# Optimization experiments

Hardware: AMD Instinct MI355X
Metric: run time of the kernel (lower is better)

The kernel has to match this reference:

```python
import jax, jax.numpy as jnp
import numpy as np

B, T, V, L = 32, 1000, 1024, 128
BLANK = 0
NEG = -1e30  # log-space -inf surrogate (fp32 safe)


def setup_inputs() -> dict:
    key = jax.random.key(0)
    k1, k2 = jax.random.split(key)
    hs_pad = jax.random.normal(k1, (B, T, V), dtype=jnp.float32)
    h_lens = jnp.full((B,), T, dtype=jnp.int32)
    ys_pad = jax.random.randint(k2, (B, L), 1, V, dtype=jnp.int32)  # blank=0 excluded
    ys_lens = jnp.full((B,), L, dtype=jnp.int32)
    return {"hs_pad": hs_pad, "h_lens": h_lens, "ys_pad": ys_pad, "ys_lens": ys_lens}


def ctc_loss(hs_pad, h_lens, ys_pad, ys_lens):
    """log_softmax + CTC forward (alpha) DP, 'mean' reduction like torch.nn.CTCLoss."""
    logp = jax.nn.log_softmax(hs_pad, axis=-1)          # (B, T, V)
    Bsz, Tm, _ = hs_pad.shape
    Lm = ys_pad.shape[1]
    S = 2 * Lm + 1                                       # extended label lattice width
    # Extended label sequence: blank, y1, blank, y2, ..., yL, blank
    ext = jnp.zeros((Bsz, S), ys_pad.dtype).at[:, 1::2].set(ys_pad)
    # Gather log-probs at extended labels: (B, T, S)
    lp_ext = jnp.take_along_axis(logp, jnp.broadcast_to(ext[:, None, :], (Bsz, Tm, S)), axis=2)
    # Skip transition s-2 -> s allowed iff ext[s] != blank and ext[s] != ext[s-2]
    ext_m2 = jnp.pad(ext, ((0, 0), (2, 0)), constant_values=BLANK)[:, :S]
    skip = (ext != BLANK) & (ext != ext_m2) & (jnp.arange(S)[None, :] >= 2)

    # alpha at t=0: only lattice positions 0 (blank) and 1 (first label)
    alpha0 = (jnp.full((Bsz, S), NEG, dtype=logp.dtype)
              .at[:, 0].set(lp_ext[:, 0, 0])
              .at[:, 1].set(lp_ext[:, 0, 1]))

    def step(alpha, xs):
        lp_t, t = xs                                     # lp_t: (B, S)
        a1 = alpha
        a2 = jnp.pad(alpha, ((0, 0), (1, 0)), constant_values=NEG)[:, :S]
        a3 = jnp.where(skip, jnp.pad(alpha, ((0, 0), (2, 0)), constant_values=NEG)[:, :S], NEG)
        new = jnp.logaddexp(jnp.logaddexp(a1, a2), a3) + lp_t
        active = (t < h_lens)[:, None]                   # freeze alpha past each h_len
        return jnp.where(active, new, alpha), None

    lp_seq = jnp.moveaxis(lp_ext, 1, 0)[1:]              # (T-1, B, S)
    ts = jnp.arange(1, Tm)
    alpha, _ = jax.lax.scan(step, alpha0, (lp_seq, ts))

    # Final log-likelihood: last blank (2*len) or last label (2*len - 1)
    idx_blank = (2 * ys_lens)[:, None]
    idx_label = (2 * ys_lens - 1)[:, None]
    a_end = jnp.logaddexp(jnp.take_along_axis(alpha, idx_blank, axis=1)[:, 0],
                          jnp.take_along_axis(alpha, idx_label, axis=1)[:, 0])
    loss = -a_end                                        # (B,)
    # torch 'mean': per-sample loss divided by target length, then batch mean
    return jnp.mean(loss / ys_lens.astype(loss.dtype))


def reference(hs_pad, h_lens, ys_pad, ys_lens):
    return ctc_loss(hs_pad, h_lens, ys_pad, ys_lens)
```

## Files before the change

kernel.cpp:

```cpp
#include <hip/hip_runtime.h>
#include <math.h>

constexpr int Bc = 32;
constexpr int Tc = 1000;
constexpr int Vc = 1024;
constexpr int Lc = 128;
constexpr int Sc = 2 * Lc + 1;
constexpr int SPq = 256;
constexpr float NEGF = -1e30f;
constexpr float L2E = 1.4426950408889634f;
constexpr float LN2 = 0.6931471805599453f;
constexpr int ENEG = -(1 << 24);

#if __has_builtin(__builtin_amdgcn_exp2f)
#define EXP2F(x) __builtin_amdgcn_exp2f(x)
#else
#define EXP2F(x) exp2f(x)
#endif
#if __has_builtin(__builtin_amdgcn_logf)
#define LOG2F(x) __builtin_amdgcn_logf(x)
#else
#define LOG2F(x) log2f(x)
#endif
#if __has_builtin(__builtin_amdgcn_ldexpf)
#define LDEXPF(x, e) __builtin_amdgcn_ldexpf(x, e)
#else
#define LDEXPF(x, e) ldexpf(x, e)
#endif
#if __has_builtin(__builtin_amdgcn_frexp_expf)
#define FREXPE(x) __builtin_amdgcn_frexp_expf(x)
#else
__device__ inline int FREXPE(float x) { int e; (void)frexpf(x, &e); return e; }
#endif

__device__ __forceinline__ float dpp_wave_shr1(float x) {
  return __int_as_float(__builtin_amdgcn_update_dpp(
      0, __float_as_int(x), 0x138 , 0xf, 0xf, true));
}
__device__ __forceinline__ int dpp_wave_shr1_i(int x) {
  return __builtin_amdgcn_update_dpp(0, x, 0x138 , 0xf, 0xf, true);
}


__global__ __launch_bounds__(256) void ctc_lse_gather(
    const float* __restrict__ hs, const int* __restrict__ ys,
    float* __restrict__ lpe, float* __restrict__ out) {
  if (blockIdx.x == 0 && threadIdx.x == 0) out[0] = 0.f;
  const int wv = threadIdx.x >> 6;
  const int lane = threadIdx.x & 63;
  const int bt = blockIdx.x * 4 + wv;
  const int b = bt / Tc;
  const float* row = hs + (size_t)bt * Vc;

  __shared__ float xs_all[4][Vc];
  float* xs = xs_all[wv];

  float4 v[4];
#pragma unroll
  for (int q = 0; q < 4; ++q) v[q] = reinterpret_cast<const float4*>(row)[lane + 64 * q];
#pragma unroll
  for (int q = 0; q < 4; ++q) { v[q].x *= L2E; v[q].y *= L2E; v[q].z *= L2E; v[q].w *= L2E; }

  float m = -3.4e38f;
#pragma unroll
  for (int q = 0; q < 4; ++q)
    m = fmaxf(m, fmaxf(fmaxf(v[q].x, v[q].y), fmaxf(v[q].z, v[q].w)));
#pragma unroll
  for (int off = 32; off; off >>= 1) m = fmaxf(m, __shfl_xor(m, off, 64));

  float sum = 0.f;
#pragma unroll
  for (int q = 0; q < 4; ++q)
    sum += EXP2F(v[q].x - m) + EXP2F(v[q].y - m) + EXP2F(v[q].z - m) + EXP2F(v[q].w - m);
#pragma unroll
  for (int off = 32; off; off >>= 1) sum += __shfl_xor(sum, off, 64);
  const float lse2 = m + LOG2F(sum);

#pragma unroll
  for (int q = 0; q < 4; ++q) reinterpret_cast<float4*>(xs)[lane + 64 * q] = v[q];
  __syncthreads();

  const int la1 = ys[b * Lc + 2 * lane];
  const int la3 = ys[b * Lc + 2 * lane + 1];
  float4 o;
  o.x = EXP2F(xs[0] - lse2);
  o.y = EXP2F(xs[la1] - lse2);
  o.z = EXP2F(xs[la3] - lse2);
  o.w = (lane == 63) ? o.x : 0.f;
  reinterpret_cast<float4*>(lpe + (size_t)bt * SPq)[lane] = o;
}

__global__ __launch_bounds__(64) void ctc_alpha(
    const float* __restrict__ lpe, const int* __restrict__ ys,
    const int* __restrict__ hlen, const int* __restrict__ ylen,
    float* __restrict__ out) {
  const int b = blockIdx.x;
  const int lane = threadIdx.x;
  const float* pb = lpe + (size_t)b * Tc * SPq;
  const float* pl = pb + lane * 4;
  const int* yb = ys + b * Lc;

  const float sk1 = (lane >= 1 && yb[2 * lane - 1] != yb[2 * lane]) ? 1.f : 0.f;
  const float sk3 = (yb[2 * lane] != yb[2 * lane + 1]) ? 1.f : 0.f;

  float m0 = (lane == 0) ? pb[0] : 0.f;
  float m1 = (lane == 0) ? pb[1] : 0.f;
  float m2 = 0.f, m3 = 0.f, m4 = 0.f;
  int E = (lane == 0) ? 0 : ENEG;
  float fsh = 0.f;

  const int Te = min(hlen[b], Tc);

  auto renorm = [&]() {
    const float mx = fmaxf(fmaxf(fmaxf(m0, m1), fmaxf(m2, m3)), m4);
    const int e = FREXPE(mx);
    const int E1 = (mx > 0.f) ? E + e : ENEG;
    int Eup = dpp_wave_shr1_i(E1);
    if (lane == 0) Eup = ENEG;
    const int En = max(E1, Eup);
    const int dm = E - En;
    fsh = LDEXPF(1.f, Eup - En);
    m0 = LDEXPF(m0, dm);
    m1 = LDEXPF(m1, dm);
    m2 = LDEXPF(m2, dm);
    m3 = LDEXPF(m3, dm);
    m4 = LDEXPF(m4, dm);
    E = En;
  };

  auto step = [&](const float4 v) {
    const float msh = dpp_wave_shr1(m3);
    const float am = msh * fsh;
    const float n0 = (m0 + am) * v.x;
    const float n1 = fmaf(sk1, am, m1 + m0) * v.y;
    const float n2 = (m2 + m1) * v.x;
    const float n3 = fmaf(sk3, m1, m3 + m2) * v.z;
    const float n4 = (m4 + m3) * v.w;
    m0 = n0; m1 = n1; m2 = n2; m3 = n3; m4 = n4;
  };

  float4 bufA[8], bufB[8], bufC[8], bufD[8];
#define LOAD8(BUF, GI)                                                        \
  do {                                                                        \
    const float* p_ = pl + (size_t)(1 + 8 * (GI)) * SPq;                      \
    _Pragma("unroll") for (int k_ = 0; k_ < 8; ++k_)                          \
        BUF[k_] = *reinterpret_cast<const float4*>(p_ + k_ * SPq);            \
    __builtin_amdgcn_sched_barrier(0);   \
  } while (0)
#define STEP8(BUF)                                                            \
  do {                                                                        \
    renorm();                                                                 \
    _Pragma("unroll") for (int k_ = 0; k_ < 8; ++k_) step(BUF[k_]);           \
  } while (0)

  const int G = (Te - 1) / 8;
  int g = 0;
  if (G > 0) LOAD8(bufA, 0);
  if (G > 1) LOAD8(bufB, 1);
  if (G > 2) LOAD8(bufC, 2);
  while (g + 4 <= G) {
    LOAD8(bufD, g + 3);
    STEP8(bufA);
    if (g + 4 < G) LOAD8(bufA, g + 4);
    STEP8(bufB);
    if (g + 5 < G) LOAD8(bufB, g + 5);
    STEP8(bufC);
    if (g + 6 < G) LOAD8(bufC, g + 6);
    STEP8(bufD);
    g += 4;
  }
  const int r = G - g;
  if (r >= 1) STEP8(bufA);
  if (r >= 2) STEP8(bufB);
  if (r >= 3) STEP8(bufC);
  {
    const int t0 = 1 + 8 * G;
    const int R = Te - t0;
#pragma unroll
    for (int k = 0; k < 7; ++k)
      if (k < R) bufD[k] = *reinterpret_cast<const float4*>(pl + (size_t)(t0 + k) * SPq);
#pragma unroll
    for (int k = 0; k < 7; ++k)
      if (k < R) { renorm(); step(bufD[k]); }
  }
#undef LOAD8
#undef STEP8

  __shared__ float msm[Sc];
  __shared__ int esm[64];
#pragma unroll
  for (int j = 0; j < 4; ++j) msm[4 * lane + j] = (j == 0 ? m0 : j == 1 ? m1 : j == 2 ? m2 : m3);
  if (lane == 63) msm[256] = m4;
  esm[lane] = E;
  __syncthreads();
  if (lane == 0) {
    const int yl = ylen[b];
    const int s1 = 2 * yl, s0 = 2 * yl - 1;
    const int l1 = (s1 == 256) ? 63 : (s1 >> 2);
    const int l0 = s0 >> 2;
    const float vx = msm[s1]; const int ex = esm[l1];
    const float vy = msm[s0]; const int ey = esm[l0];
    const int Em = max(ex, ey);
    const float rr = LDEXPF(vx, ex - Em) + LDEXPF(vy, ey - Em);
    const float ae2 = (rr > 0.f) ? (LOG2F(rr) + (float)Em) : NEGF;
    atomicAdd(out, -(ae2 * LN2) / ((float)yl * (float)Bc));
  }
}

extern "C" void kernel_launch(void* const* d_in, const int* in_sizes, int n_in,
                              void* d_out, int out_size, void* d_ws, size_t ws_size,
                              hipStream_t stream) {
  const float* hs = (const float*)d_in[0];
  const int* hlen = (const int*)d_in[1];
  const int* ys = (const int*)d_in[2];
  const int* ylen = (const int*)d_in[3];
  float* out = (float*)d_out;

  float* lpe = (float*)d_ws;

  ctc_lse_gather<<<Bc * Tc / 4, 256, 0, stream>>>(hs, ys, lpe, out);
  ctc_alpha<<<Bc, 64, 0, stream>>>(lpe, ys, hlen, ylen, out);
}
```

Baseline: 238.5 us.

## Stream alpha-DP inputs through an LDS ring via async global_load_lds

The register-held four-buffer prefetch in the alpha recursion kernel is replaced by a 5-slot shared-memory ring. Each slot is filled with async global-to-LDS loads, and explicit vmcnt waits keep up to four groups of 8 timesteps in flight. The aim is to free VGPRs and keep memory latency hidden behind the serial DP chain. In exchange it adds an LDS read on every step, and the wait counts have to stay matched to the issued loads. The ring is reused with no explicit barrier, which holds only because each block is a single wave.

```diff
diff --git a/kernel.cpp b/kernel.cpp
--- a/kernel.cpp
+++ b/kernel.cpp
@@ -41,6 +41,13 @@
   return __builtin_amdgcn_update_dpp(0, x, 0x138 , 0xf, 0xf, true);
 }
 
+__device__ __forceinline__ void gload_lds16(const float* g, float* l) {
+  __builtin_amdgcn_global_load_lds(
+      (const __attribute__((address_space(1))) void*)g,
+      (__attribute__((address_space(3))) void*)l, 16, 0, 0);
+}
+#define WAITV(n) asm volatile("s_waitcnt vmcnt(" #n ")" ::: "memory")
+
 
 __global__ __launch_bounds__(256) void ctc_lse_gather(
     const float* __restrict__ hs, const int* __restrict__ ys,
@@ -99,6 +106,8 @@
   const float* pb = lpe + (size_t)b * Tc * SPq;
   const float* pl = pb + lane * 4;
   const int* yb = ys + b * Lc;
+
+  __shared__ float ring[5][8][SPq];
 
   const float sk1 = (lane >= 1 && yb[2 * lane - 1] != yb[2 * lane]) ? 1.f : 0.f;
   const float sk3 = (yb[2 * lane] != yb[2 * lane + 1]) ? 1.f : 0.f;
@@ -139,52 +148,46 @@
     m0 = n0; m1 = n1; m2 = n2; m3 = n3; m4 = n4;
   };
 
-  float4 bufA[8], bufB[8], bufC[8], bufD[8];
-#define LOAD8(BUF, GI)                                                        \
-  do {                                                                        \
-    const float* p_ = pl + (size_t)(1 + 8 * (GI)) * SPq;                      \
-    _Pragma("unroll") for (int k_ = 0; k_ < 8; ++k_)                          \
-        BUF[k_] = *reinterpret_cast<const float4*>(p_ + k_ * SPq);            \
-    __builtin_amdgcn_sched_barrier(0);   \
-  } while (0)
-#define STEP8(BUF)                                                            \
-  do {                                                                        \
-    renorm();                                                                 \
-    _Pragma("unroll") for (int k_ = 0; k_ < 8; ++k_) step(BUF[k_]);           \
-  } while (0)
+  auto issue8 = [&](int gi) {
+    const int s = gi % 5;
+    const float* p_ = pl + (size_t)(1 + 8 * gi) * SPq;
+#pragma unroll
+    for (int k = 0; k < 8; ++k)
+      gload_lds16(p_ + (size_t)k * SPq, &ring[s][k][0]);
+  };
+  auto step8 = [&](int g) {
+    const int s = g % 5;
+    renorm();
+#pragma unroll
+    for (int k = 0; k < 8; ++k) {
+      const float4 v = reinterpret_cast<const float4*>(&ring[s][k][0])[lane];
+      step(v);
+    }
+  };
 
   const int G = (Te - 1) / 8;
-  int g = 0;
-  if (G > 0) LOAD8(bufA, 0);
-  if (G > 1) LOAD8(bufB, 1);
-  if (G > 2) LOAD8(bufC, 2);
-  while (g + 4 <= G) {
-    LOAD8(bufD, g + 3);
-    STEP8(bufA);
-    if (g + 4 < G) LOAD8(bufA, g + 4);
-    STEP8(bufB);
-    if (g + 5 < G) LOAD8(bufB, g + 5);
-    STEP8(bufC);
-    if (g + 6 < G) LOAD8(bufC, g + 6);
-    STEP8(bufD);
-    g += 4;
+  int issued = 0;
+  for (; issued < G && issued < 4; ++issued) issue8(issued);
+  for (int g = 0; g < G; ++g) {
+    const int inflight = issued - g;
+    if (inflight >= 4)      WAITV(24);
+    else if (inflight == 3) WAITV(16);
+    else if (inflight == 2) WAITV(8);
+    else                    WAITV(0);
+    if (issued < G) { issue8(issued); ++issued; }
+    step8(g);
   }
-  const int r = G - g;
-  if (r >= 1) STEP8(bufA);
-  if (r >= 2) STEP8(bufB);
-  if (r >= 3) STEP8(bufC);
   {
     const int t0 = 1 + 8 * G;
     const int R = Te - t0;
+    float4 bt[7];
 #pragma unroll
     for (int k = 0; k < 7; ++k)
-      if (k < R) bufD[k] = *reinterpret_cast<const float4*>(pl + (size_t)(t0 + k) * SPq);
+      if (k < R) bt[k] = *reinterpret_cast<const float4*>(pl + (size_t)(t0 + k) * SPq);
 #pragma unroll
     for (int k = 0; k < 7; ++k)
-      if (k < R) { renorm(); step(bufD[k]); }
+      if (k < R) { renorm(); step(bt[k]); }
   }
-#undef LOAD8
-#undef STEP8
 
   __shared__ float msm[Sc];
   __shared__ int esm[64];
```

After: 272.6 us. +14.3%, slower.
